# Kernel tuning notes

Measured on AMD Instinct MI355X. Metric: run time of the kernel, lower is better.

The kernel has to match this reference:

```python
import jax, jax.numpy as jnp
from jax import lax
import numpy as np

VOCAB, TAGS, EMBED, HIDDEN, BATCH, SEQ = 50000, 9, 300, 1000, 32, 200


def setup_inputs() -> dict:
    key = jax.random.key(0)
    ks = jax.random.split(key, 12)
    s_e = 1.0 / np.sqrt(HIDDEN)
    inp = {
        "x": jax.random.randint(ks[0], (SEQ, BATCH), 0, VOCAB),
        "y": jax.random.randint(ks[1], (SEQ, BATCH), 0, TAGS),
        "embed_w": jax.random.normal(ks[2], (VOCAB, EMBED), jnp.float32),
        "W_ih": jax.random.uniform(ks[3], (4 * HIDDEN, EMBED), jnp.float32, -s_e, s_e),
        "W_hh": jax.random.uniform(ks[4], (4 * HIDDEN, HIDDEN), jnp.float32, -s_e, s_e),
        "b_ih": jax.random.uniform(ks[5], (4 * HIDDEN,), jnp.float32, -s_e, s_e),
        "b_hh": jax.random.uniform(ks[6], (4 * HIDDEN,), jnp.float32, -s_e, s_e),
        "lin_w": jax.random.uniform(ks[7], (TAGS, HIDDEN), jnp.float32, -s_e, s_e),
        "lin_b": jax.random.uniform(ks[8], (TAGS,), jnp.float32, -s_e, s_e),
        "start_trans": jax.random.uniform(ks[9], (TAGS,), jnp.float32, -0.1, 0.1),
        "end_trans": jax.random.uniform(ks[10], (TAGS,), jnp.float32, -0.1, 0.1),
        "trans": jax.random.uniform(ks[11], (TAGS, TAGS), jnp.float32, -0.1, 0.1),
    }
    return inp


def _forward(x, y, embed_w, W_ih, W_hh, b_ih, b_hh, lin_w, lin_b, start_trans, end_trans, trans):
    T, B = x.shape
    H = W_hh.shape[1]
    embeds = embed_w[x]  # [T,B,E]
    # Precompute input contribution to gates: [T,B,4H]
    xg = jnp.einsum("tbe,ge->tbg", embeds, W_ih) + b_ih + b_hh

    def lstm_step(carry, xg_t):
        h, c = carry
        g = xg_t + h @ W_hh.T  # [B,4H]
        i, f, gg, o = jnp.split(g, 4, axis=-1)  # PyTorch gate order i,f,g,o
        c = jax.nn.sigmoid(f) * c + jax.nn.sigmoid(i) * jnp.tanh(gg)
        h = jax.nn.sigmoid(o) * jnp.tanh(c)
        return (h, c), h

    h0 = jnp.zeros((B, H), embeds.dtype)
    _, hs = lax.scan(lstm_step, (h0, h0), xg)  # hs: [T,B,H]

    tag_space = jnp.einsum("tbh,kh->tbk", hs, lin_w) + lin_b  # [T,B,K]
    # Faithful to original: log_softmax over dim=1 (the batch axis)
    emissions = jax.nn.log_softmax(tag_space, axis=1)

    # ---- CRF log-likelihood (pytorch-crf semantics, full mask, sum reduction) ----
    b_idx = jnp.arange(B)
    em_at_y = jnp.take_along_axis(emissions, y[:, :, None], axis=2)[:, :, 0]  # [T,B]
    numerator = (
        start_trans[y[0]]
        + em_at_y.sum(axis=0)
        + trans[y[:-1], y[1:]].sum(axis=0)
        + end_trans[y[-1]]
    )  # [B]

    alpha0 = start_trans[None, :] + emissions[0]  # [B,K]

    def crf_step(alpha, em_t):
        # alpha: [B,K] over previous tag; em_t: [B,K]
        nxt = jax.nn.logsumexp(alpha[:, :, None] + trans[None, :, :] + em_t[:, None, :], axis=1)
        return nxt, None

    alpha, _ = lax.scan(crf_step, alpha0, emissions[1:])
    log_z = jax.nn.logsumexp(alpha + end_trans[None, :], axis=1)  # [B]
    return (numerator - log_z).sum()


def reference(x, y, embed_w, W_ih, W_hh, b_ih, b_hh, lin_w, lin_b, start_trans, end_trans, trans):
    return _forward(x, y, embed_w, W_ih, W_hh, b_ih, b_hh, lin_w, lin_b, start_trans, end_trans, trans)
```

## Files before the change

kernel.cpp:

```cpp
#include <hip/hip_runtime.h>

#define T_SEQ 200
#define NB    32
#define NE    300
#define NH    1000
#define NK    9
#define NJ    4096
#define EPD   320
#define WSCALE 256.0f
#define HSCALE 16.0f
#define LSCALE 512.0f
#define GSCALE (1.0f / (256.0f * 16.0f))
#define TSCALE (1.0f / (16.0f * 512.0f))

typedef __attribute__((ext_vector_type(4))) float f32x4;
typedef __attribute__((ext_vector_type(8))) short s16x8;
typedef __attribute__((ext_vector_type(4))) short s16x4;
typedef unsigned long long u64;

__device__ __forceinline__ unsigned short f2bf(float f) {
    union { float f; unsigned u; } v; v.f = f;
    unsigned r = v.u + 0x7FFFu + ((v.u >> 16) & 1u);
    return (unsigned short)(r >> 16);
}
__device__ __forceinline__ float bf2f(unsigned short h) {
    union { unsigned u; float f; } v; v.u = ((unsigned)h) << 16;
    return v.f;
}
__device__ __forceinline__ float ftanh(float x) {
    float e = __expf(fminf(2.f * x, 80.f));
    return (e - 1.f) / (e + 1.f);
}
__device__ __forceinline__ float fsig(float x) {
    return 1.f / (1.f + __expf(-x));
}
__device__ __forceinline__ unsigned nt_poll(const unsigned* p) {
    unsigned r;
    asm volatile("global_load_dword %0, %1, off nt\n\t"
                 "s_waitcnt vmcnt(0)"
                 : "=v"(r) : "v"(p) : "memory");
    return r;
}
__device__ __forceinline__ void plain_pub(unsigned* p, unsigned v) {
    __hip_atomic_store(p, v, __ATOMIC_RELAXED, __HIP_MEMORY_SCOPE_WORKGROUP);
}

__global__ __launch_bounds__(256) void prep_all(
    const int* __restrict__ x, const float* __restrict__ embed_w,
    const float* __restrict__ W_ih, const float* __restrict__ b_ih,
    const float* __restrict__ b_hh, const float* __restrict__ lin_w,
    unsigned short* __restrict__ emb_bf, unsigned short* __restrict__ wih_bf,
    float* __restrict__ biasg, unsigned char* __restrict__ linw_q,
    unsigned* __restrict__ ctrl)
{
    const int blk = blockIdx.x, tid = threadIdx.x;
    if (blk < T_SEQ) {
        const int t = blk;
        if (blk == 0) {
            for (int i = tid; i < 2048; i += 256)
                ctrl[i] = (i == 497) ? 0xffffffffu : 0u;
        }
        for (int idx = tid; idx < NB * EPD; idx += 256) {
            int b = idx / EPD, e = idx - b * EPD;
            float v = (e < NE) ? embed_w[(size_t)x[t * NB + b] * NE + e] : 0.f;
            emb_bf[((size_t)t * NB + b) * EPD + e] = f2bf(v);
        }
        return;
    }
    const int b2 = blk - T_SEQ;
    for (int idx = tid; idx < 64 * EPD; idx += 256) {
        int jr = idx / EPD, e = idx - jr * EPD;
        int jp = b2 * 64 + jr;
        int wgu = jp >> 7, rr = jp & 127, g = rr >> 5, uu = rr & 31;
        int m = wgu * 32 + uu;
        float v = (m < NH && e < NE) ? W_ih[(size_t)(g * NH + m) * NE + e] : 0.f;
        wih_bf[(size_t)jp * EPD + e] = f2bf(v);
    }
    if (tid < 64) {
        int jp = b2 * 64 + tid;
        int wgu = jp >> 7, rr = jp & 127, g = rr >> 5, uu = rr & 31;
        int m = wgu * 32 + uu;
        biasg[jp] = (m < NH) ? (b_ih[g * NH + m] + b_hh[g * NH + m]) : 0.f;
    }
    if (b2 < 16) {
        int n = b2, k = tid * 4;
        float v0 = (n < NK && k + 0 < NH) ? lin_w[(size_t)n * NH + k + 0] * LSCALE : 0.f;
        float v1 = (n < NK && k + 1 < NH) ? lin_w[(size_t)n * NH + k + 1] * LSCALE : 0.f;
        float v2 = (n < NK && k + 2 < NH) ? lin_w[(size_t)n * NH + k + 2] * LSCALE : 0.f;
        float v3 = (n < NK && k + 3 < NH) ? lin_w[(size_t)n * NH + k + 3] * LSCALE : 0.f;
        int p01 = __builtin_amdgcn_cvt_pk_fp8_f32(v0, v1, 0, false);
        int p23 = __builtin_amdgcn_cvt_pk_fp8_f32(v2, v3, 0, false);
        ((unsigned*)linw_q)[n * 256 + tid] =
            ((unsigned)p01 & 0xffffu) | ((unsigned)p23 << 16);
    }
}

__device__ __forceinline__ int gate_xg(unsigned* done, int ready, int tn, int lane) {
    while (ready <= tn) {
        unsigned v = 64u;
        if (lane < 8 && ready + lane < T_SEQ)
            v = __hip_atomic_load(&done[ready + lane], __ATOMIC_RELAXED,
                                  __HIP_MEMORY_SCOPE_AGENT);
        unsigned m = (unsigned)__ballot((int)(v >= 64u)) & 255u;
        if (m & 1u) {
            unsigned run = (m == 255u) ? 8u : (unsigned)__builtin_ctz(~m);
            ready += (int)run;
        } else {
            __builtin_amdgcn_s_sleep(1);
        }
    }
    return ready;
}

__global__ __launch_bounds__(256, 1) void lstm_kernel(
    const float* __restrict__ W_hh,
    const unsigned short* __restrict__ emb_bf,
    const unsigned short* __restrict__ wih_bf,
    const float* __restrict__ biasg,
    unsigned short* __restrict__ xg,
    unsigned char* __restrict__ h_q,
    unsigned* __restrict__ ctrl)
{
    __shared__ __align__(16) unsigned char s_w[128 * 1024];
    __shared__ int s_chunk, s_grp, s_pid, s_mode;

    const int tid = threadIdx.x;

    if (tid == 0) {
        unsigned xcc;
        asm volatile("s_getreg_b32 %0, hwreg(HW_REG_XCC_ID)" : "=s"(xcc));
        xcc &= 15u;
        unsigned myidx = __hip_atomic_fetch_add(&ctrl[480 + xcc], 1u,
                             __ATOMIC_RELAXED, __HIP_MEMORY_SCOPE_AGENT);
        __threadfence();
        unsigned tot = __hip_atomic_fetch_add(&ctrl[496], 1u,
                             __ATOMIC_RELAXED, __HIP_MEMORY_SCOPE_AGENT);
        if (tot == 255u) {
            __threadfence();
            unsigned w0 = 0xffu, w1 = 0xffu;
            for (unsigned xx = 0; xx < 16; ++xx) {
                unsigned cx = __hip_atomic_load(&ctrl[480 + xx], __ATOMIC_RELAXED,
                                                __HIP_MEMORY_SCOPE_AGENT);
                if (cx >= 32u) {
                    if (w0 == 0xffu) w0 = xx;
                    else { w1 = xx; break; }
                }
            }
            __hip_atomic_store(&ctrl[497], w0 | (w1 << 8), __ATOMIC_RELAXED,
                               __HIP_MEMORY_SCOPE_AGENT);
        }
        unsigned win;
        do {
            win = __hip_atomic_load(&ctrl[497], __ATOMIC_RELAXED,
                                    __HIP_MEMORY_SCOPE_AGENT);
        } while (win == 0xffffffffu);
        unsigned w0 = win & 0xffu, w1 = (win >> 8) & 0xffu;
        int grp = -1;
        if (xcc == w0 && myidx < 32u) grp = 0;
        else if (xcc == w1 && myidx < 32u) grp = 1;
        s_grp = grp;
        s_chunk = (grp >= 0) ? (int)myidx : -1;
        s_pid = (grp >= 0) ? -1
                     : (int)__hip_atomic_fetch_add(&ctrl[498], 1u,
                           __ATOMIC_RELAXED, __HIP_MEMORY_SCOPE_AGENT);
    }
    __syncthreads();
    const int chunk = s_chunk;
    const int w = tid >> 6, lane = tid & 63;
    const int col = lane & 15, quad = lane >> 4;
    unsigned* done = ctrl + 256;

    if (chunk < 0) {
        const int pid = s_pid;
        for (int g = pid; g < T_SEQ * 64; g += 192) {
            const int t = g >> 6, jt = g & 63;
            const unsigned short* eb = emb_bf + (size_t)t * NB * EPD;
            const unsigned short* wb = wih_bf + (size_t)(jt * 64 + w * 16 + col) * EPD;
            const unsigned short* ea0 = eb + (size_t)col * EPD;
            const unsigned short* ea1 = eb + (size_t)(16 + col) * EPD;

            f32x4 acc0 = {0.f, 0.f, 0.f, 0.f};
            f32x4 acc1 = {0.f, 0.f, 0.f, 0.f};
#pragma unroll
            for (int kc = 0; kc < EPD / 32; ++kc) {
                int ko = kc * 32 + quad * 8;
                s16x8 a0 = *(const s16x8*)&ea0[ko];
                s16x8 a1 = *(const s16x8*)&ea1[ko];
                s16x8 bb = *(const s16x8*)&wb[ko];
                acc0 = __builtin_amdgcn_mfma_f32_16x16x32_bf16(a0, bb, acc0, 0, 0, 0);
                acc1 = __builtin_amdgcn_mfma_f32_16x16x32_bf16(a1, bb, acc1, 0, 0, 0);
            }
            const int jp = jt * 64 + w * 16 + col;
            const float bi = biasg[jp];
            size_t base = ((size_t)t * NJ + jp) * NB;
            union { s16x4 v; u64 q; } p0, p1;
#pragma unroll
            for (int r = 0; r < 4; ++r) {
                p0.v[r] = (short)f2bf(acc0[r] + bi);
                p1.v[r] = (short)f2bf(acc1[r] + bi);
            }
            __hip_atomic_store((u64*)&xg[base + quad * 4], p0.q,
                               __ATOMIC_RELAXED, __HIP_MEMORY_SCOPE_AGENT);
            __hip_atomic_store((u64*)&xg[base + 16 + quad * 4], p1.q,
                               __ATOMIC_RELAXED, __HIP_MEMORY_SCOPE_AGENT);
            __syncthreads();
            if (tid == 0)
                __hip_atomic_fetch_add(&done[t], 1u, __ATOMIC_RELAXED,
                                       __HIP_MEMORY_SCOPE_AGENT);
        }
        return;
    }

    const int grp = s_grp;
    const size_t GOFF = (size_t)grp * 16384;
    unsigned* slowf = ctrl + grp * 64;
    unsigned* fastf = ctrl + 128 + grp * 64;
    unsigned* s_w32 = (unsigned*)s_w;

    for (int idx = tid; idx < 128 * 256; idx += 256) {
        int r = idx >> 8, dw = idx & 255;
        int g = r >> 5, uu = r & 31, m = chunk * 32 + uu;
        float4 w4 = make_float4(0.f, 0.f, 0.f, 0.f);
        if (m < NH && dw < 250)
            w4 = *(const float4*)&W_hh[(size_t)(g * NH + m) * NH + dw * 4];
        int p0 = __builtin_amdgcn_cvt_pk_fp8_f32(w4.x * WSCALE, w4.y * WSCALE, 0, false);
        int p1 = __builtin_amdgcn_cvt_pk_fp8_f32(w4.z * WSCALE, w4.w * WSCALE, 0, false);
        unsigned v = ((unsigned)p0 & 0xffffu) | ((unsigned)p1 << 16);
        int kb = dw >> 1;
        int kbs = kb ^ (r & 15);
        s_w32[r * 256 + (kbs << 1) + (dw & 1)] = v;
    }
    if (tid < 128)
        *(unsigned*)(h_q + GOFF + (size_t)chunk * 512 + tid * 4) = 0u;
    __syncthreads();
    if (tid == 0) {
        plain_pub(&fastf[chunk * 2 + 0], 1u);
        plain_pub(&fastf[chunk * 2 + 1], 1u);
        __hip_atomic_store(&slowf[chunk * 2 + 0], 1u, __ATOMIC_RELAXED,
                           __HIP_MEMORY_SCOPE_AGENT);
        __hip_atomic_store(&slowf[chunk * 2 + 1], 1u, __ATOMIC_RELAXED,
                           __HIP_MEMORY_SCOPE_AGENT);
    }
    if (grp == 0 && chunk == 0 && w == 0) {
        int md = 2;
        for (int it = 0; it < 8192; ++it) {
            unsigned v = nt_poll(&fastf[lane]);
            if (__all((int)(v >= 1u))) { md = 1; break; }
        }
        if (lane == 0) {
            __hip_atomic_store(&ctrl[499], (unsigned)md, __ATOMIC_RELAXED,
                               __HIP_MEMORY_SCOPE_AGENT);
            s_mode = md;
        }
    } else if (tid == 0) {
        unsigned m;
        do {
            m = __hip_atomic_load(&ctrl[499], __ATOMIC_RELAXED,
                                  __HIP_MEMORY_SCOPE_AGENT);
        } while (m == 0u);
        s_mode = (int)m;
    }
    __syncthreads();
    const int mode = s_mode;

    if (w >= 2) return;
    const int p = w;
    const int fid = chunk * 2 + w;

    int ready = gate_xg(done, 0, 1, lane);
    s16x4 xcur[4], xnxt[4];
#pragma unroll
    for (int g = 0; g < 4; ++g)
        xcur[g] = *(const s16x4*)&xg[((size_t)0 * NJ + chunk * 128 + (2 * g + p) * 16 + col) * NB
                                     + grp * 16 + quad * 4];

    float c[4] = {0.f, 0.f, 0.f, 0.f};
    const int rw = quad * 4;
    const int boff = col * 32 + quad * 8;

    for (int t = 0; t < T_SEQ; ++t) {
        const unsigned need = (unsigned)(t + 1);
        const int gt = t + 2;
        bool gate_pending = (gt < T_SEQ) && (ready <= gt);
        if (mode == 1) {
            for (;;) {
                unsigned v = nt_poll(&fastf[lane]);
                bool hok = __all((int)(v >= need));
                if (gate_pending) {
                    unsigned d = 64u;
                    if (lane < 8 && ready + lane < T_SEQ)
                        d = __hip_atomic_load(&done[ready + lane], __ATOMIC_RELAXED,
                                              __HIP_MEMORY_SCOPE_AGENT);
                    unsigned m = (unsigned)__ballot((int)(d >= 64u)) & 255u;
                    if (m & 1u)
                        ready += (m == 255u) ? 8 : (int)__builtin_ctz(~m);
                    gate_pending = (ready <= gt);
                }
                if (hok && !gate_pending) break;
            }
        } else {
            for (;;) {
                unsigned v = __hip_atomic_load(&slowf[lane], __ATOMIC_RELAXED,
                                               __HIP_MEMORY_SCOPE_AGENT);
                bool hok = __all((int)(v >= need));
                if (gate_pending) {
                    unsigned d = 64u;
                    if (lane < 8 && ready + lane < T_SEQ)
                        d = __hip_atomic_load(&done[ready + lane], __ATOMIC_RELAXED,
                                              __HIP_MEMORY_SCOPE_AGENT);
                    unsigned m = (unsigned)__ballot((int)(d >= 64u)) & 255u;
                    if (m & 1u)
                        ready += (m == 255u) ? 8 : (int)__builtin_ctz(~m);
                    gate_pending = (ready <= gt);
                }
                if (hok && !gate_pending) break;
            }
        }
        asm volatile("" ::: "memory");

        const unsigned char* pb = h_q + (size_t)t * 32768 + GOFF + boff;
        u64 a[32];
#pragma unroll
        for (int kc = 0; kc < 32; ++kc)
            a[kc] = *(const u64*)(pb + (size_t)kc * 512);

        if (t + 1 < T_SEQ) {
#pragma unroll
            for (int g = 0; g < 4; ++g)
                xnxt[g] = *(const s16x4*)&xg[((size_t)(t + 1) * NJ + chunk * 128 + (2 * g + p) * 16 + col) * NB
                                             + grp * 16 + quad * 4];
        }

        f32x4 acc0 = {0.f, 0.f, 0.f, 0.f};
        f32x4 acc1 = {0.f, 0.f, 0.f, 0.f};
        f32x4 acc2 = {0.f, 0.f, 0.f, 0.f};
        f32x4 acc3 = {0.f, 0.f, 0.f, 0.f};
#pragma unroll
        for (int kc = 0; kc < 32; ++kc) {
            int kb = kc * 4 + quad;
            u64 b0 = *(const u64*)&s_w[((0 * 2 + p) * 16 + col) * 1024 + ((kb ^ col) << 3)];
            u64 b1 = *(const u64*)&s_w[((1 * 2 + p) * 16 + col) * 1024 + ((kb ^ col) << 3)];
            u64 b2 = *(const u64*)&s_w[((2 * 2 + p) * 16 + col) * 1024 + ((kb ^ col) << 3)];
            u64 b3 = *(const u64*)&s_w[((3 * 2 + p) * 16 + col) * 1024 + ((kb ^ col) << 3)];
            acc0 = __builtin_amdgcn_mfma_f32_16x16x32_fp8_fp8((long)a[kc], (long)b0, acc0, 0, 0, 0);
            acc1 = __builtin_amdgcn_mfma_f32_16x16x32_fp8_fp8((long)a[kc], (long)b1, acc1, 0, 0, 0);
            acc2 = __builtin_amdgcn_mfma_f32_16x16x32_fp8_fp8((long)a[kc], (long)b2, acc2, 0, 0, 0);
            acc3 = __builtin_amdgcn_mfma_f32_16x16x32_fp8_fp8((long)a[kc], (long)b3, acc3, 0, 0, 0);
        }

        float hv[4];
#pragma unroll
        for (int r = 0; r < 4; ++r) {
            float gi = acc0[r] * GSCALE + bf2f((unsigned short)xcur[0][r]);
            float gf = acc1[r] * GSCALE + bf2f((unsigned short)xcur[1][r]);
            float gg = acc2[r] * GSCALE + bf2f((unsigned short)xcur[2][r]);
            float go = acc3[r] * GSCALE + bf2f((unsigned short)xcur[3][r]);
            c[r] = fsig(gf) * c[r] + fsig(gi) * ftanh(gg);
            hv[r] = fsig(go) * ftanh(c[r]);
        }
        {
            int p01 = __builtin_amdgcn_cvt_pk_fp8_f32(hv[0] * HSCALE, hv[1] * HSCALE, 0, false);
            int p23 = __builtin_amdgcn_cvt_pk_fp8_f32(hv[2] * HSCALE, hv[3] * HSCALE, 0, false);
            unsigned char* pg = h_q + (size_t)(t + 1) * 32768 + GOFF + (size_t)chunk * 512
                              + p * 16 + col;
            pg[(rw + 0) * 32] = (unsigned char)(p01 & 0xff);
            pg[(rw + 1) * 32] = (unsigned char)((p01 >> 8) & 0xff);
            pg[(rw + 2) * 32] = (unsigned char)(p23 & 0xff);
            pg[(rw + 3) * 32] = (unsigned char)((p23 >> 8) & 0xff);
        }
        asm volatile("s_waitcnt vmcnt(0)" ::: "memory");
        if (lane == 0) {
            plain_pub(&fastf[fid], (unsigned)(t + 2));
            if (mode == 2)
                __hip_atomic_store(&slowf[fid], (unsigned)(t + 2),
                                   __ATOMIC_RELAXED, __HIP_MEMORY_SCOPE_AGENT);
        }
#pragma unroll
        for (int g = 0; g < 4; ++g) xcur[g] = xnxt[g];
    }
}

__global__ __launch_bounds__(512) void tagem_crf(
    const unsigned char* __restrict__ h_q,
    const unsigned char* __restrict__ linw_q,
    const float* __restrict__ lin_b,
    const int* __restrict__ y,
    const float* __restrict__ start_trans, const float* __restrict__ end_trans,
    const float* __restrict__ trans,
    float* __restrict__ em, unsigned* __restrict__ ctrl,
    float* __restrict__ out)
{
    __shared__ float s_ts[NB * NK];
    __shared__ float s_lse[NK];
    __shared__ float s_trans[NK * NK];
    __shared__ float s_red[NB];
    __shared__ int   s_y[T_SEQ * NB];
    const int blk = blockIdx.x, tid = threadIdx.x;
    unsigned* pflag = ctrl + 512;

    if (blk < T_SEQ) {
        const int t = blk;
        const int w = tid >> 6, lane = tid & 63;
        const int col = lane & 15, quad = lane >> 4;
        if (w < 2) {
            const unsigned char* pa = h_q + (size_t)(t + 1) * 32768 + (size_t)w * 16384
                                    + col * 32 + quad * 8;
            const unsigned char* pw = linw_q + (size_t)col * 1024 + quad * 8;
            f32x4 acc = {0.f, 0.f, 0.f, 0.f};
#pragma unroll 8
            for (int kc = 0; kc < 32; ++kc) {
                u64 a  = *(const u64*)(pa + (size_t)kc * 512);
                u64 bv = *(const u64*)(pw + kc * 32);
                acc = __builtin_amdgcn_mfma_f32_16x16x32_fp8_fp8((long)a, (long)bv, acc, 0, 0, 0);
            }
            if (col < NK) {
                float lb = lin_b[col];
#pragma unroll
                for (int r = 0; r < 4; ++r)
                    s_ts[(w * 16 + quad * 4 + r) * NK + col] = acc[r] * TSCALE + lb;
            }
        }
        __syncthreads();
        if (tid < NK) {
            float m = -1e30f;
            for (int bb = 0; bb < NB; ++bb) m = fmaxf(m, s_ts[bb * NK + tid]);
            float s = 0.f;
            for (int bb = 0; bb < NB; ++bb) s += __expf(s_ts[bb * NK + tid] - m);
            s_lse[tid] = m + __logf(s);
        }
        __syncthreads();
        if (tid < NB * NK) {
            int k = tid - (tid / NK) * NK;
            union { float f; unsigned u; } cv;
            cv.f = s_ts[tid] - s_lse[k];
            __hip_atomic_store((unsigned*)em + (size_t)t * NB * NK + tid, cv.u,
                               __ATOMIC_RELAXED, __HIP_MEMORY_SCOPE_AGENT);
        }
        asm volatile("s_waitcnt vmcnt(0)" ::: "memory");
        __syncthreads();
        if (tid == 0) {
            __threadfence();
            __hip_atomic_store(&pflag[t], 1u, __ATOMIC_RELAXED,
                               __HIP_MEMORY_SCOPE_AGENT);
        }
        return;
    }

    const int gb = tid >> 4;
    const int q  = tid & 15;
    const int lane = tid & 63;
    const int gbase = lane & 48;

    if (tid < NK * NK) s_trans[tid] = trans[tid];
    for (int i = tid; i < T_SEQ * NB; i += 512) s_y[i] = y[i];
    __syncthreads();

    auto wait_pages = [&](int base) {
        for (;;) {
            unsigned v = 1u;
            if (lane < 8 && base + lane < T_SEQ)
                v = __hip_atomic_load(&pflag[base + lane], __ATOMIC_RELAXED,
                                      __HIP_MEMORY_SCOPE_AGENT);
            if (__all((int)(v >= 1u))) break;
            __builtin_amdgcn_s_sleep(2);
        }
    };
    auto emload = [&](int t) -> float {
        union { unsigned u; float f; } cv;
        cv.u = __hip_atomic_load((const unsigned*)em + (size_t)(t * NB + gb) * NK + q,
                                 __ATOMIC_RELAXED, __HIP_MEMORY_SCOPE_AGENT);
        return cv.f;
    };

    float trC[NK];
#pragma unroll
    for (int i = 0; i < NK; ++i)
        trC[i] = (q < NK) ? s_trans[i * NK + q] : 0.f;

    wait_pages(0);
    wait_pages(8);

    float emv0 = (q < NK) ? emload(0) : -1e30f;
    int yp = s_y[gb];
    float num = start_trans[yp] + __shfl(emv0, gbase | yp, 64);
    float alpha = (q < NK) ? (start_trans[q] + emv0) : -1e30f;

    float e[8];
#pragma unroll
    for (int j = 0; j < 8; ++j) {
        int t = 1 + j;
        e[j] = (q < NK && t < T_SEQ) ? emload(t) : -1e30f;
    }
    for (int blk2 = 0; blk2 < 25; ++blk2) {
        float enx[8];
        const int tb = 1 + (blk2 + 1) * 8;
        wait_pages(tb);
#pragma unroll
        for (int j = 0; j < 8; ++j) {
            int t = tb + j;
            enx[j] = (q < NK && t < T_SEQ) ? emload(t) : -1e30f;
        }
#pragma unroll
        for (int j = 0; j < 8; ++j) {
            int t = 1 + blk2 * 8 + j;
            if (t < T_SEQ) {
                float ev = e[j];
                int yc = s_y[t * NB + gb];
                num += s_trans[yp * NK + yc] + __shfl(ev, gbase | yc, 64);
                yp = yc;
                float a_i[NK];
#pragma unroll
                for (int i = 0; i < NK; ++i)
                    a_i[i] = __shfl(alpha, gbase | i, 64) + trC[i];
                float m = a_i[0];
#pragma unroll
                for (int i = 1; i < NK; ++i) m = fmaxf(m, a_i[i]);
                float s = 0.f;
#pragma unroll
                for (int i = 0; i < NK; ++i) s += __expf(a_i[i] - m);
                alpha = (q < NK) ? (ev + m + __logf(s)) : -1e30f;
            }
        }
#pragma unroll
        for (int j = 0; j < 8; ++j) e[j] = enx[j];
    }

    num += end_trans[yp];
    float v = (q < NK) ? (alpha + end_trans[q]) : -1e30f;
    float mg = v;
#pragma unroll
    for (int off = 8; off >= 1; off >>= 1)
        mg = fmaxf(mg, __shfl_xor(mg, off, 64));
    float sg = __expf(v - mg);
#pragma unroll
    for (int off = 8; off >= 1; off >>= 1)
        sg += __shfl_xor(sg, off, 64);
    float lz = mg + __logf(sg);
    if (q == 0) s_red[gb] = num - lz;
    __syncthreads();
    if (tid == 0) {
        float tot = 0.f;
        for (int i = 0; i < NB; ++i) tot += s_red[i];
        out[0] = tot;
    }
}

extern "C" void kernel_launch(void* const* d_in, const int* in_sizes, int n_in,
                              void* d_out, int out_size, void* d_ws, size_t ws_size,
                              hipStream_t stream)
{
    const int*   x           = (const int*)d_in[0];
    const int*   y           = (const int*)d_in[1];
    const float* embed_w     = (const float*)d_in[2];
    const float* W_ih        = (const float*)d_in[3];
    const float* W_hh        = (const float*)d_in[4];
    const float* b_ih        = (const float*)d_in[5];
    const float* b_hh        = (const float*)d_in[6];
    const float* lin_w       = (const float*)d_in[7];
    const float* lin_b       = (const float*)d_in[8];
    const float* start_trans = (const float*)d_in[9];
    const float* end_trans   = (const float*)d_in[10];
    const float* trans       = (const float*)d_in[11];
    float* out = (float*)d_out;

    char* ws = (char*)d_ws;
    unsigned short* xg     = (unsigned short*)(ws);
    unsigned char*  h_q    = (unsigned char*)(ws + 52428800);
    unsigned char*  linw_q = (unsigned char*)(ws + 59015168);
    float*          em     = (float*)(ws + 65601536);
    unsigned*       ctrl   = (unsigned*)(ws + 65831936);
    float*          biasg  = (float*)(ws + 65840128);
    unsigned short* emb_bf = (unsigned short*)(ws + 65856512);
    unsigned short* wih_bf = (unsigned short*)(ws + 69952512);

    prep_all<<<dim3(T_SEQ + 64), 256, 0, stream>>>(x, embed_w, W_ih, b_ih, b_hh,
                                                   lin_w, emb_bf, wih_bf, biasg,
                                                   linw_q, ctrl);

    lstm_kernel<<<dim3(256), 256, 0, stream>>>(W_hh, emb_bf, wih_bf, biasg,
                                               xg, h_q, ctrl);

    tagem_crf<<<dim3(T_SEQ + 1), 512, 0, stream>>>(h_q, linw_q, lin_b, y,
                                                   start_trans, end_trans, trans,
                                                   em, ctrl, out);
}
```

Measured before the change: 949.5 us.

## Split recurrent matmul wait into halves to overlap with partial flag readiness

New measurement: 1.099 ms. +15.7%, slower.

```diff
diff --git a/kernel.cpp b/kernel.cpp
--- a/kernel.cpp
+++ b/kernel.cpp
@@ -282,10 +282,11 @@
         const unsigned need = (unsigned)(t + 1);
         const int gt = t + 2;
         bool gate_pending = (gt < T_SEQ) && (ready <= gt);
+        bool half2_ready = false;
         if (mode == 1) {
             for (;;) {
                 unsigned v = nt_poll(&fastf[lane]);
-                bool hok = __all((int)(v >= need));
+                u64 bal = __ballot((int)(v >= need));
                 if (gate_pending) {
                     unsigned d = 64u;
                     if (lane < 8 && ready + lane < T_SEQ)
@@ -296,13 +297,16 @@
                         ready += (m == 255u) ? 8 : (int)__builtin_ctz(~m);
                     gate_pending = (ready <= gt);
                 }
-                if (hok && !gate_pending) break;
+                if ((unsigned)bal == 0xffffffffu && !gate_pending) {
+                    half2_ready = ((unsigned)(bal >> 32) == 0xffffffffu);
+                    break;
+                }
             }
         } else {
             for (;;) {
                 unsigned v = __hip_atomic_load(&slowf[lane], __ATOMIC_RELAXED,
                                                __HIP_MEMORY_SCOPE_AGENT);
-                bool hok = __all((int)(v >= need));
+                u64 bal = __ballot((int)(v >= need));
                 if (gate_pending) {
                     unsigned d = 64u;
                     if (lane < 8 && ready + lane < T_SEQ)
@@ -313,7 +317,10 @@
                         ready += (m == 255u) ? 8 : (int)__builtin_ctz(~m);
                     gate_pending = (ready <= gt);
                 }
-                if (hok && !gate_pending) break;
+                if ((unsigned)bal == 0xffffffffu && !gate_pending) {
+                    half2_ready = ((unsigned)(bal >> 32) == 0xffffffffu);
+                    break;
+                }
             }
         }
         asm volatile("" ::: "memory");
@@ -321,22 +328,57 @@
         const unsigned char* pb = h_q + (size_t)t * 32768 + GOFF + boff;
         u64 a[32];
 #pragma unroll
-        for (int kc = 0; kc < 32; ++kc)
+        for (int kc = 0; kc < 16; ++kc)
             a[kc] = *(const u64*)(pb + (size_t)kc * 512);
-
-        if (t + 1 < T_SEQ) {
-#pragma unroll
-            for (int g = 0; g < 4; ++g)
-                xnxt[g] = *(const s16x4*)&xg[((size_t)(t + 1) * NJ + chunk * 128 + (2 * g + p) * 16 + col) * NB
-                                             + grp * 16 + quad * 4];
-        }
 
         f32x4 acc0 = {0.f, 0.f, 0.f, 0.f};
         f32x4 acc1 = {0.f, 0.f, 0.f, 0.f};
         f32x4 acc2 = {0.f, 0.f, 0.f, 0.f};
         f32x4 acc3 = {0.f, 0.f, 0.f, 0.f};
 #pragma unroll
-        for (int kc = 0; kc < 32; ++kc) {
+        for (int kc = 0; kc < 16; ++kc) {
+            int kb = kc * 4 + quad;
+            u64 b0 = *(const u64*)&s_w[((0 * 2 + p) * 16 + col) * 1024 + ((kb ^ col) << 3)];
+            u64 b1 = *(const u64*)&s_w[((1 * 2 + p) * 16 + col) * 1024 + ((kb ^ col) << 3)];
+            u64 b2 = *(const u64*)&s_w[((2 * 2 + p) * 16 + col) * 1024 + ((kb ^ col) << 3)];
+            u64 b3 = *(const u64*)&s_w[((3 * 2 + p) * 16 + col) * 1024 + ((kb ^ col) << 3)];
+            acc0 = __builtin_amdgcn_mfma_f32_16x16x32_fp8_fp8((long)a[kc], (long)b0, acc0, 0, 0, 0);
+            acc1 = __builtin_amdgcn_mfma_f32_16x16x32_fp8_fp8((long)a[kc], (long)b1, acc1, 0, 0, 0);
+            acc2 = __builtin_amdgcn_mfma_f32_16x16x32_fp8_fp8((long)a[kc], (long)b2, acc2, 0, 0, 0);
+            acc3 = __builtin_amdgcn_mfma_f32_16x16x32_fp8_fp8((long)a[kc], (long)b3, acc3, 0, 0, 0);
+        }
+
+        if (!half2_ready) {
+            if (mode == 1) {
+                for (;;) {
+                    unsigned v = (lane >= 32) ? nt_poll(&fastf[lane]) : need;
+                    if (__all((int)(v >= need))) break;
+                }
+            } else {
+                for (;;) {
+                    unsigned v = (lane >= 32)
+                        ? __hip_atomic_load(&slowf[lane], __ATOMIC_RELAXED,
+                                            __HIP_MEMORY_SCOPE_AGENT)
+                        : need;
+                    if (__all((int)(v >= need))) break;
+                }
+            }
+            asm volatile("" ::: "memory");
+        }
+
+#pragma unroll
+        for (int kc = 16; kc < 32; ++kc)
+            a[kc] = *(const u64*)(pb + (size_t)kc * 512);
+
+        if (t + 1 < T_SEQ) {
+#pragma unroll
+            for (int g = 0; g < 4; ++g)
+                xnxt[g] = *(const s16x4*)&xg[((size_t)(t + 1) * NJ + chunk * 128 + (2 * g + p) * 16 + col) * NB
+                                             + grp * 16 + quad * 4];
+        }
+
+#pragma unroll
+        for (int kc = 16; kc < 32; ++kc) {
             int kb = kc * 4 + quad;
             u64 b0 = *(const u64*)&s_w[((0 * 2 + p) * 16 + col) * 1024 + ((kb ^ col) << 3)];
             u64 b1 = *(const u64*)&s_w[((1 * 2 + p) * 16 + col) * 1024 + ((kb ^ col) << 3)];
```
